# Performance work log

Measured on AMD Instinct MI355X. Metric: run time of the kernel, lower is better.

Reference implementation:

```python
import jax, jax.numpy as jnp
import numpy as np

B, S, D_MODEL, D_K, D_V = 8, 2048, 1024, 1024, 1024


def setup_inputs() -> dict:
    key = jax.random.key(0)
    ks = jax.random.split(key, 10)
    scale = 1.0 / np.sqrt(D_MODEL)
    return {
        "inputs_q": jax.random.normal(ks[0], (B, S, D_MODEL), dtype=jnp.float32),
        "inputs_k": jax.random.normal(ks[1], (B, S, D_MODEL), dtype=jnp.float32),
        "inputs_v": jax.random.normal(ks[2], (B, S, D_MODEL), dtype=jnp.float32),
        "mask": jax.random.randint(ks[3], (B, S), 0, 2, dtype=jnp.int32),
        "Wq": jax.random.normal(ks[4], (D_MODEL, D_K), dtype=jnp.float32) * scale,
        "bq": jnp.zeros((D_K,), dtype=jnp.float32),
        "Wk": jax.random.normal(ks[5], (D_MODEL, D_K), dtype=jnp.float32) * scale,
        "bk": jnp.zeros((D_K,), dtype=jnp.float32),
        "Wv": jax.random.normal(ks[6], (D_MODEL, D_V), dtype=jnp.float32) * scale,
        "bv": jnp.zeros((D_V,), dtype=jnp.float32),
    }


def reference(inputs_q, inputs_k, inputs_v, mask, Wq, bq, Wk, bk, Wv, bv):
    # Dense projections: [B,S,d_model] @ [d_model,d] + bias
    q = jnp.einsum("bsd,dk->bsk", inputs_q, Wq) + bq
    k = jnp.einsum("bsd,dk->bsk", inputs_k, Wk) + bk
    v = jnp.einsum("bsd,dv->bsv", inputs_v, Wv) + bv
    # scaled dot-product scores [B,S,S]
    scores = jnp.einsum("bqk,bsk->bqs", q, k) / jnp.sqrt(jnp.float32(D_K))
    # padding mask [B,S] -> matrix mask via min(row, col); 1 = valid
    m = mask.astype(jnp.float32)
    matrix_mask = jnp.minimum(m[:, :, None], m[:, None, :])  # [B,S,S]
    mask_float = 1.0 - matrix_mask  # 1 where masked
    scores = scores + mask_float * (-1e9)
    attention_weights = jax.nn.softmax(scores, axis=-1)
    out = jnp.einsum("bqs,bsv->bqv", attention_weights, v)  # [B,S,d_v]
    return out
```

## Files before the change

kernel.cpp:

```cpp
#include <hip/hip_runtime.h>
#include <stdint.h>


typedef unsigned short u16;
typedef __attribute__((ext_vector_type(8))) short short8;
typedef __attribute__((ext_vector_type(4))) float f32x4;

__device__ __forceinline__ u16 f2bf(float x) {
  unsigned u = __float_as_uint(x);
  return (u16)((u + 0x7FFFu + ((u >> 16) & 1u)) >> 16);
}
__device__ __forceinline__ float bf2f(u16 h) {
  return __uint_as_float(((unsigned)h) << 16);
}

__device__ __forceinline__ void stage16(const void* g, void* l) {
  const __attribute__((address_space(1))) uint32_t* gp =
      (const __attribute__((address_space(1))) uint32_t*)(uintptr_t)g;
  __attribute__((address_space(3))) uint32_t* lp =
      (__attribute__((address_space(3))) uint32_t*)(uintptr_t)l;
  __builtin_amdgcn_global_load_lds(gp, lp, 16, 0, 0);
}

__device__ __forceinline__ short8 ld8(const char* p, int off) {
  return *(const short8*)(p + off);
}

__global__ __launch_bounds__(256) void maskscan(const int* __restrict__ mask,
                                                int* __restrict__ idxA,
                                                int* __restrict__ nvA,
                                                int* __restrict__ nvp128A) {
  const int b = blockIdx.x;
  const int t = threadIdx.x, lane = t & 63, w = t >> 6;
  const int* m = mask + b * 2048;
  int v[8], loc = 0;
#pragma unroll
  for (int i = 0; i < 8; ++i) { v[i] = m[t * 8 + i]; loc += v[i]; }
  int sc = loc;
  for (int off = 1; off < 64; off <<= 1) {
    int n = __shfl_up(sc, off);
    if (lane >= off) sc += n;
  }
  __shared__ int wsum[4];
  if (lane == 63) wsum[w] = sc;
  __syncthreads();
  int woff = 0;
  for (int i = 0; i < w; ++i) woff += wsum[i];
  int pos = woff + sc - loc;
#pragma unroll
  for (int i = 0; i < 8; ++i)
    if (v[i]) idxA[b * 2048 + (pos++)] = t * 8 + i;
  if (t == 255) {
    const int nv = woff + sc;
    nvA[b] = nv;
    nvp128A[b] = (nv + 127) & ~127;
  }
}

__global__ __launch_bounds__(256) void compact3(const float* __restrict__ Xq,
                                                const float* __restrict__ Xk,
                                                const float* __restrict__ Xv,
                                                const int* __restrict__ idxA,
                                                const int* __restrict__ nvA,
                                                u16* __restrict__ Oq,
                                                u16* __restrict__ Ok,
                                                u16* __restrict__ Ov) {
  const int b = blockIdx.y, j = blockIdx.x, z = blockIdx.z;
  if (j >= nvA[b]) return;
  const float* X = (z == 0) ? Xq : (z == 1) ? Xk : Xv;
  u16* out = (z == 0) ? Oq : (z == 1) ? Ok : Ov;
  const int src = idxA[b * 2048 + j];
  const float4* s = (const float4*)(X + ((size_t)b * 2048 + src) * 1024);
  ushort4* d = (ushort4*)(out + ((size_t)b * 2048 + j) * 1024);
  const float4 f = s[threadIdx.x];
  ushort4 o;
  o.x = f2bf(f.x); o.y = f2bf(f.y); o.z = f2bf(f.z); o.w = f2bf(f.w);
  d[threadIdx.x] = o;
}

__global__ __launch_bounds__(256) void wtcol(const float* __restrict__ Wq,
                                             const float* __restrict__ Wk,
                                             const float* __restrict__ Wv,
                                             u16* __restrict__ WT,
                                             const float* __restrict__ Xv,
                                             float* __restrict__ partial) {
  const int bid = blockIdx.x;
  const int t = threadIdx.x;
  if (bid < 3072) {
    __shared__ float tile[32][33];
    const int z = bid >> 10;
    const int xy = bid & 1023;
    const int n0 = (xy & 31) * 32, d0 = (xy >> 5) * 32;
    const float* W = (z == 0) ? Wq : (z == 1) ? Wk : Wv;
    u16* out = WT + (size_t)z * 1024 * 1024;
    const int tx = t & 31, ty = t >> 5;
#pragma unroll
    for (int i = 0; i < 4; ++i)
      tile[ty + 8 * i][tx] = W[(size_t)(d0 + ty + 8 * i) * 1024 + n0 + tx];
    __syncthreads();
#pragma unroll
    for (int i = 0; i < 4; ++i)
      out[(size_t)(n0 + ty + 8 * i) * 1024 + d0 + tx] = f2bf(tile[tx][ty + 8 * i]);
  } else {
    const int r = bid - 3072;
    const int b = r & 7, dq = (r >> 3) & 3, sck = r >> 5;
    const int d = dq * 256 + t;
    const float* p = Xv + ((size_t)b * 2048 + sck * 256) * 1024 + d;
    float s0 = 0, s1 = 0, s2 = 0, s3 = 0;
    for (int rr = 0; rr < 256; rr += 4) {
      s0 += p[(size_t)(rr + 0) * 1024];
      s1 += p[(size_t)(rr + 1) * 1024];
      s2 += p[(size_t)(rr + 2) * 1024];
      s3 += p[(size_t)(rr + 3) * 1024];
    }
    partial[((size_t)b * 8 + sck) * 1024 + d] = (s0 + s1) + (s2 + s3);
  }
}

__global__ __launch_bounds__(256) void vpartk(const float* __restrict__ partial,
                                              const float* __restrict__ Wv,
                                              float* __restrict__ vpart) {
  const int b = blockIdx.x, cq = blockIdx.y, dk = blockIdx.z;
  const int t = threadIdx.x;
  __shared__ float mx[128];
  if (t < 128) {
    const int d = dk * 128 + t;
    float m = 0;
#pragma unroll
    for (int i = 0; i < 8; ++i) m += partial[((size_t)b * 8 + i) * 1024 + d];
    mx[t] = m * (1.0f / 2048.0f);
  }
  __syncthreads();
  const int c = cq * 256 + t;
  const float* wp = Wv + (size_t)(dk * 128) * 1024 + c;
  float acc = 0;
#pragma unroll 4
  for (int i = 0; i < 128; ++i) acc += mx[i] * wp[(size_t)i * 1024];
  vpart[((size_t)b * 8 + dk) * 1024 + c] = acc;
}

__global__ __launch_bounds__(256) void vmeanred(const float* __restrict__ vpart,
                                                const float* __restrict__ bv,
                                                float* __restrict__ vmean) {
  const int b = blockIdx.x;
  const int c = blockIdx.y * 256 + threadIdx.x;
  float acc = bv[c];
#pragma unroll
  for (int i = 0; i < 8; ++i) acc += vpart[((size_t)b * 8 + i) * 1024 + c];
  vmean[b * 1024 + c] = acc;
}

__global__ __launch_bounds__(256) void bcast(const int* __restrict__ mask,
                                             const float* __restrict__ vmean,
                                             float* __restrict__ out) {
  const int b = blockIdx.y, row = blockIdx.x;
  if (mask[b * 2048 + row] != 0) return;
  const float4 vv = ((const float4*)(vmean + b * 1024))[threadIdx.x];
  ((float4*)(out + ((size_t)b * 2048 + row) * 1024))[threadIdx.x] = vv;
}

#define BAR __builtin_amdgcn_s_barrier()
#define SB __builtin_amdgcn_sched_barrier(0)
#define LGK0 asm volatile("s_waitcnt lgkmcnt(0)" ::: "memory")
#define VM4 asm volatile("s_waitcnt vmcnt(4)" ::: "memory")
#define VM0 asm volatile("s_waitcnt vmcnt(0)" ::: "memory")

#define RDA4(P0, P1, MH)                                      \
  {                                                           \
    _Pragma("unroll") for (int mf_ = 0; mf_ < 4; ++mf_) {     \
      afr[0][mf_] = ld8(P0, (MH) * 8192 + mf_ * 2048);        \
      afr[1][mf_] = ld8(P1, (MH) * 8192 + mf_ * 2048);        \
    }                                                         \
  }

#define RDB2(DST, P0, P1, NH)                                 \
  {                                                           \
    DST[0][0] = ld8(P0, (NH) * 4096);                         \
    DST[0][1] = ld8(P0, (NH) * 4096 + 2048);                  \
    DST[1][0] = ld8(P1, (NH) * 4096);                         \
    DST[1][1] = ld8(P1, (NH) * 4096 + 2048);                  \
  }

#define MQ16(ACC, NH, BF)                                                \
  __builtin_amdgcn_s_setprio(1);                                         \
  {                                                                      \
    _Pragma("unroll") for (int ks_ = 0; ks_ < 2; ++ks_)                  \
        _Pragma("unroll") for (int mf_ = 0; mf_ < 4; ++mf_)              \
            _Pragma("unroll") for (int nf_ = 0; nf_ < 2; ++nf_)          \
                ACC[mf_][(NH) * 2 + nf_] =                               \
                    __builtin_amdgcn_mfma_f32_16x16x32_bf16(             \
                        afr[ks_][mf_], BF[ks_][nf_],                     \
                        ACC[mf_][(NH) * 2 + nf_], 0, 0, 0);              \
  }                                                                      \
  __builtin_amdgcn_s_setprio(0);

__global__ __launch_bounds__(512, 2) void gemm8p(
    const u16* __restrict__ A, const u16* __restrict__ B,
    void* __restrict__ C, void* __restrict__ C1, void* __restrict__ C2,
    const float* __restrict__ b0, const float* __restrict__ b1,
    const float* __restrict__ b2,
    const int* __restrict__ nvp128A,
    int K, int lda, int ldb, int ldc) {
  __shared__ __attribute__((aligned(16))) char smem[131072];
  const int tid = threadIdx.x;
  const int lane = tid & 63;
  const int w = tid >> 6;
  const int wr = w >> 2;
  const int wc = w & 3;

  const int bx = blockIdx.x;
  const int z = bx & 7;
  int r = bx >> 3;
  const int o = r >> 5; r &= 31;
  const int bm = r >> 2, bn = r & 3;

  const int nvp = nvp128A[z];
  if (bm * 256 >= nvp) return;

  const u16* Ap = A + (size_t)o * (8u * 2048u * 1024u) + (size_t)z * (2048u * 1024u);
  const u16* Bp = B + (size_t)o * (1024u * 1024u);
  const int half = K >> 7;

  const int srow = w * 8 + (lane >> 3);
  const int scol = ((lane & 7) ^ (lane >> 3)) << 3;
  const u16* Ab0 = Ap + (size_t)(bm * 256 + srow) * lda + scol;
  const u16* Ab1 = Ab0 + (size_t)64 * lda;
  const u16* Ab2 = Ab0 + (size_t)128 * lda;
  const u16* Ab3 = Ab0 + (size_t)192 * lda;
  const u16* Bb0 = Bp + (size_t)(bn * 256 + srow) * ldb + scol;
  const u16* Bb1 = Bb0 + (size_t)64 * ldb;
  const u16* Bb2 = Bb0 + (size_t)128 * ldb;
  const u16* Bb3 = Bb0 + (size_t)192 * ldb;
  char* ldsW = smem + w * 1024;

  const int fr = lane & 15;
  const int fq = lane >> 4;
  const int fx = (fr & 7) << 4;
  const char* pak0 = smem + wr * 16384 + fr * 128 + ((fq * 16) ^ fx);
  const char* pak1 = smem + wr * 16384 + fr * 128 + ((64 + fq * 16) ^ fx);
  const char* pak0b = pak0 + 65536;
  const char* pak1b = pak1 + 65536;
  const char* pbk0 = smem + 32768 + wc * 8192 + fr * 128 + ((fq * 16) ^ fx);
  const char* pbk1 = smem + 32768 + wc * 8192 + fr * 128 + ((64 + fq * 16) ^ fx);
  const char* pbk0b = pbk0 + 65536;
  const char* pbk1b = pbk1 + 65536;

  f32x4 acc0[4][4] = {};
  f32x4 acc1[4][4] = {};
  short8 afr[2][4], bf0[2][2], bf1[2][2];

  stage16(Bb0, ldsW + 32768); stage16(Bb1, ldsW + 40960);
  stage16(Bb2, ldsW + 49152); stage16(Bb3, ldsW + 57344);
  stage16(Ab0, ldsW + 0);     stage16(Ab1, ldsW + 8192);
  stage16(Ab2, ldsW + 16384); stage16(Ab3, ldsW + 24576);
  stage16(Bb0 + 64, ldsW + 98304);  stage16(Bb1 + 64, ldsW + 106496);
  stage16(Bb2 + 64, ldsW + 114688); stage16(Bb3 + 64, ldsW + 122880);
  VM4;
  BAR;

  int koff = 0;
  for (int i = 0; i < half - 1; ++i) {
    const int o1 = koff + 64, o2 = koff + 128, o3 = koff + 192;
    RDA4(pak0, pak1, 0); RDB2(bf0, pbk0, pbk1, 0);
    stage16(Ab0 + o1, ldsW + 65536); stage16(Ab1 + o1, ldsW + 73728);
    SB; BAR; LGK0; MQ16(acc0, 0, bf0); BAR;
    RDB2(bf1, pbk0, pbk1, 1);
    stage16(Ab2 + o1, ldsW + 81920); stage16(Ab3 + o1, ldsW + 90112);
    SB; BAR; LGK0; MQ16(acc0, 1, bf1); BAR;
    RDA4(pak0, pak1, 1);
    stage16(Bb0 + o2, ldsW + 32768); stage16(Bb1 + o2, ldsW + 40960);
    SB; BAR; LGK0; MQ16(acc1, 0, bf0); BAR;
    stage16(Bb2 + o2, ldsW + 49152); stage16(Bb3 + o2, ldsW + 57344);
    SB; BAR; MQ16(acc1, 1, bf1); VM4; BAR;
    RDA4(pak0b, pak1b, 0); RDB2(bf0, pbk0b, pbk1b, 0);
    stage16(Ab0 + o2, ldsW + 0); stage16(Ab1 + o2, ldsW + 8192);
    SB; BAR; LGK0; MQ16(acc0, 0, bf0); BAR;
    RDB2(bf1, pbk0b, pbk1b, 1);
    stage16(Ab2 + o2, ldsW + 16384); stage16(Ab3 + o2, ldsW + 24576);
    SB; BAR; LGK0; MQ16(acc0, 1, bf1); BAR;
    RDA4(pak0b, pak1b, 1);
    stage16(Bb0 + o3, ldsW + 98304); stage16(Bb1 + o3, ldsW + 106496);
    SB; BAR; LGK0; MQ16(acc1, 0, bf0); BAR;
    stage16(Bb2 + o3, ldsW + 114688); stage16(Bb3 + o3, ldsW + 122880);
    SB; BAR; MQ16(acc1, 1, bf1); VM4; BAR;
    koff += 128;
  }
  {
    const int o1 = koff + 64;
    RDA4(pak0, pak1, 0); RDB2(bf0, pbk0, pbk1, 0);
    stage16(Ab0 + o1, ldsW + 65536); stage16(Ab1 + o1, ldsW + 73728);
    SB; BAR; LGK0; MQ16(acc0, 0, bf0); BAR;
    RDB2(bf1, pbk0, pbk1, 1);
    stage16(Ab2 + o1, ldsW + 81920); stage16(Ab3 + o1, ldsW + 90112);
    SB; BAR; LGK0; MQ16(acc0, 1, bf1); BAR;
    RDA4(pak0, pak1, 1);
    SB; BAR; LGK0; MQ16(acc1, 0, bf0); BAR;
    SB; BAR; MQ16(acc1, 1, bf1); VM0; BAR;
    RDA4(pak0b, pak1b, 0); RDB2(bf0, pbk0b, pbk1b, 0);
    SB; BAR; LGK0; MQ16(acc0, 0, bf0); BAR;
    RDB2(bf1, pbk0b, pbk1b, 1);
    SB; BAR; LGK0; MQ16(acc0, 1, bf1); BAR;
    RDA4(pak0b, pak1b, 1);
    SB; BAR; LGK0; MQ16(acc1, 0, bf0); BAR;
    SB; BAR; MQ16(acc1, 1, bf1); BAR;
  }

  const int colb = bn * 256 + wc * 64 + fr;
#pragma unroll
  for (int mh = 0; mh < 2; ++mh) {
    f32x4(&ac)[4][4] = mh ? acc1 : acc0;
    const int rowl = bm * 256 + wr * 128 + mh * 64 + fq * 4;
    if (o < 2) {
      const float* bp = o ? b1 : b0;
      u16* Cb = (u16*)(o ? C1 : C) + (size_t)z * (2048u * 1024u);
#pragma unroll
      for (int mf = 0; mf < 4; ++mf)
#pragma unroll
        for (int n = 0; n < 4; ++n) {
          const int c = colb + n * 16;
          const float bv = bp[c];
#pragma unroll
          for (int j = 0; j < 4; ++j)
            Cb[(size_t)(rowl + mf * 16 + j) * ldc + c] = f2bf(ac[mf][n][j] + bv);
        }
    } else {
      u16* Cb = (u16*)C2;
#pragma unroll
      for (int mf = 0; mf < 4; ++mf) {
        const int s_ = rowl + mf * 16;
#pragma unroll
        for (int n = 0; n < 4; ++n) {
          const int c = colb + n * 16;
          const float bv = b2[c];
          ushort4 ov;
          ov.x = f2bf(ac[mf][n][0] + bv);
          ov.y = f2bf(ac[mf][n][1] + bv);
          ov.z = f2bf(ac[mf][n][2] + bv);
          ov.w = f2bf(ac[mf][n][3] + bv);
          *(ushort4*)&Cb[((size_t)z * 1024 + c) * 2048 + s_] = ov;
        }
      }
    }
  }
}

template <int MODE>
__global__ __launch_bounds__(256, 2) void gemm128(
    const u16* __restrict__ A, const u16* __restrict__ B, void* __restrict__ C,
    const int* __restrict__ nvp128A, const int* __restrict__ nvA,
    const int* __restrict__ idxA,
    int K, int lda, int ldb, int ldc,
    size_t Az, size_t Bz, size_t Cz) {
  __shared__ __attribute__((aligned(16))) u16 lsA[2 * 128 * 32];
  __shared__ __attribute__((aligned(16))) u16 lsB[2 * 128 * 32];
  const int tid = threadIdx.x;
  const int lane = tid & 63;
  const int w = tid >> 6;
  const int wr = w >> 1, wc = w & 1;

  const int bx = blockIdx.x;
  const int z = bx & 7;
  const int r = bx >> 3;
  int bm, bn;
  if constexpr (MODE == 2) { bm = r >> 4; bn = r & 15; }
  else                     { bm = r >> 3; bn = r & 7; }

  const int nvp = nvp128A[z];
  if (bm * 128 >= nvp) return;
  if constexpr (MODE == 2) { if (bn * 128 >= nvp) return; }
  const int Kz = (MODE == 3) ? nvp : K;

  const u16* Ap = A + (size_t)z * Az;
  const u16* Bp = B + (size_t)z * Bz;

  const int srow = lane >> 2;
  const int scol = (lane & 3) * 8;
  const u16* Ag0 = Ap + (size_t)(bm * 128 + w * 32 + srow) * lda + scol;
  const u16* Ag1 = Ag0 + (size_t)16 * lda;
  const u16* Bg0 = Bp + (size_t)(bn * 128 + w * 32 + srow) * ldb + scol;
  const u16* Bg1 = Bg0 + (size_t)16 * ldb;
  u16* lA0 = &lsA[(w * 32) * 32];
  u16* lA1 = &lsA[(w * 32 + 16) * 32];
  u16* lB0 = &lsB[(w * 32) * 32];
  u16* lB1 = &lsB[(w * 32 + 16) * 32];

  const int arow = wr * 64 + (lane & 15);
  const int brow = wc * 64 + (lane & 15);
  const int ko = (lane >> 4) * 8;

  f32x4 acc[4][4] = {};

  auto compute = [&](int cur) {
    const u16* sA = lsA + cur * 4096;
    const u16* sB = lsB + cur * 4096;
    short8 af[4], bfr[4];
#pragma unroll
    for (int m = 0; m < 4; ++m)
      af[m] = *(const short8*)&sA[(arow + m * 16) * 32 + ko];
#pragma unroll
    for (int n = 0; n < 4; ++n)
      bfr[n] = *(const short8*)&sB[(brow + n * 16) * 32 + ko];
#pragma unroll
    for (int m = 0; m < 4; ++m)
#pragma unroll
      for (int n = 0; n < 4; ++n)
        acc[m][n] =
            __builtin_amdgcn_mfma_f32_16x16x32_bf16(af[m], bfr[n], acc[m][n], 0, 0, 0);
  };

  stage16(Ag0, lA0);
  stage16(Ag1, lA1);
  stage16(Bg0, lB0);
  stage16(Bg1, lB1);
  __syncthreads();

  int cur = 0;
  int k0 = 0;
  for (; k0 + 32 < Kz; k0 += 32) {
    const int off = (cur ^ 1) * 4096;
    const int kn = k0 + 32;
    stage16(Ag0 + kn, lA0 + off);
    stage16(Ag1 + kn, lA1 + off);
    stage16(Bg0 + kn, lB0 + off);
    stage16(Bg1 + kn, lB1 + off);
    compute(cur);
    __syncthreads();
    cur ^= 1;
  }
  compute(cur);

  const int col0 = bn * 128 + wc * 64 + (lane & 15);
  const int row0 = bm * 128 + wr * 64 + ((lane >> 4) << 2);

  if constexpr (MODE == 2) {
    u16* Cb = (u16*)C + (size_t)z * Cz;
#pragma unroll
    for (int m = 0; m < 4; ++m)
#pragma unroll
      for (int n = 0; n < 4; ++n) {
        const int c = col0 + n * 16;
#pragma unroll
        for (int j = 0; j < 4; ++j)
          Cb[(size_t)(row0 + m * 16 + j) * ldc + c] =
              f2bf(acc[m][n][j] * 0.03125f);
      }
  } else {
    const int nv = nvA[z];
    const int* idxp = idxA + z * 2048;
    float* Ob = (float*)C;
#pragma unroll
    for (int m = 0; m < 4; ++m)
#pragma unroll
      for (int j = 0; j < 4; ++j) {
        const int rowc = row0 + m * 16 + j;
        if (rowc < nv) {
          const int gr = idxp[rowc];
          float* orow = Ob + ((size_t)z * 2048 + gr) * 1024;
#pragma unroll
          for (int n = 0; n < 4; ++n) orow[col0 + n * 16] = acc[m][n][j];
        }
      }
  }
}

__global__ __launch_bounds__(256) void softmaxc(u16* __restrict__ scores,
                                                const int* __restrict__ nvA,
                                                const int* __restrict__ nvp128A) {
  const int b = blockIdx.y, row = blockIdx.x;
  const int nv = nvA[b];
  if (row >= nv) return;
  const int nvp = nvp128A[b];
  const int t = threadIdx.x, lane = t & 63, w = t >> 6;
  u16* sc = scores + ((size_t)b * 2048 + row) * 2048;
  const int c0 = t * 8;
  float v[8];
  if (c0 < nvp) {
    const ushort4 h0 = *(const ushort4*)&sc[c0];
    const ushort4 h1 = *(const ushort4*)&sc[c0 + 4];
    v[0] = bf2f(h0.x); v[1] = bf2f(h0.y); v[2] = bf2f(h0.z); v[3] = bf2f(h0.w);
    v[4] = bf2f(h1.x); v[5] = bf2f(h1.y); v[6] = bf2f(h1.z); v[7] = bf2f(h1.w);
  } else {
#pragma unroll
    for (int i = 0; i < 8; ++i) v[i] = 0.f;
  }
  float lmax = -3.0e38f;
#pragma unroll
  for (int i = 0; i < 8; ++i)
    if (c0 + i < nv) lmax = fmaxf(lmax, v[i]);
#pragma unroll
  for (int off = 32; off >= 1; off >>= 1) lmax = fmaxf(lmax, __shfl_xor(lmax, off));
  __shared__ float red[8];
  if (lane == 0) red[w] = lmax;
  __syncthreads();
  const float bmax = fmaxf(fmaxf(red[0], red[1]), fmaxf(red[2], red[3]));
  float e[8];
  float lsum = 0.f;
#pragma unroll
  for (int i = 0; i < 8; ++i) {
    e[i] = (c0 + i < nv) ? __expf(v[i] - bmax) : 0.f;
    lsum += e[i];
  }
#pragma unroll
  for (int off = 32; off >= 1; off >>= 1) lsum += __shfl_xor(lsum, off);
  if (lane == 0) red[4 + w] = lsum;
  __syncthreads();
  const float inv = 1.0f / ((red[4] + red[5]) + (red[6] + red[7]));
  if (c0 < nvp) {
    ushort4 o0, o1;
    o0.x = f2bf(e[0] * inv); o0.y = f2bf(e[1] * inv);
    o0.z = f2bf(e[2] * inv); o0.w = f2bf(e[3] * inv);
    o1.x = f2bf(e[4] * inv); o1.y = f2bf(e[5] * inv);
    o1.z = f2bf(e[6] * inv); o1.w = f2bf(e[7] * inv);
    *(ushort4*)&sc[c0] = o0;
    *(ushort4*)&sc[c0 + 4] = o1;
  }
}

extern "C" void kernel_launch(void* const* d_in, const int* in_sizes, int n_in,
                              void* d_out, int out_size, void* d_ws, size_t ws_size,
                              hipStream_t stream) {
  const float* in_q = (const float*)d_in[0];
  const float* in_k = (const float*)d_in[1];
  const float* in_v = (const float*)d_in[2];
  const int* mask = (const int*)d_in[3];
  const float* Wq = (const float*)d_in[4];
  const float* bq = (const float*)d_in[5];
  const float* Wk = (const float*)d_in[6];
  const float* bk = (const float*)d_in[7];
  const float* Wv = (const float*)d_in[8];
  const float* bv = (const float*)d_in[9];

  char* ws = (char*)d_ws;
  const size_t SZ = (size_t)16384 * 1024 * 2;
  u16* qc = (u16*)(ws);
  u16* kc = (u16*)(ws + SZ);
  u16* vcT = (u16*)(ws + 2 * SZ);
  u16* Xc = (u16*)(ws + 3 * SZ);
  u16* Xqc = Xc;
  u16* Xkc = Xc + (size_t)8 * 2048 * 1024;
  u16* Xvc = Xkc + (size_t)8 * 2048 * 1024;
  u16* scores = (u16*)(ws + 3 * SZ);
  u16* WT = (u16*)(ws + 6 * SZ);
  char* misc = ws + 6 * SZ + 6 * 1024 * 1024;
  int* idxA = (int*)misc;
  int* nvA = idxA + 8 * 2048;
  int* nvp128A = nvA + 8;
  float* partial = (float*)(misc + 128 * 1024);
  float* vmean = (float*)(misc + 384 * 1024);
  float* vpart = (float*)(misc + 448 * 1024);

  maskscan<<<8, 256, 0, stream>>>(mask, idxA, nvA, nvp128A);

  compact3<<<dim3(2048, 8, 3), 256, 0, stream>>>(in_q, in_k, in_v, idxA, nvA,
                                                 Xqc, Xkc, Xvc);
  wtcol<<<3328, 256, 0, stream>>>(Wq, Wk, Wv, WT, in_v, partial);
  vpartk<<<dim3(8, 4, 8), 256, 0, stream>>>(partial, Wv, vpart);
  vmeanred<<<dim3(8, 4), 256, 0, stream>>>(vpart, bv, vmean);

  gemm8p<<<768, 512, 0, stream>>>(
      Xqc, WT, qc, kc, vcT, bq, bk, bv, nvp128A, 1024, 1024, 1024, 1024);

  gemm128<2><<<2048, 256, 0, stream>>>(
      qc, kc, scores, nvp128A, nvA, idxA, 1024, 1024, 1024, 2048,
      (size_t)2048 * 1024, (size_t)2048 * 1024, (size_t)2048 * 2048);

  softmaxc<<<dim3(2048, 8), 256, 0, stream>>>(scores, nvA, nvp128A);

  gemm128<3><<<1024, 256, 0, stream>>>(
      scores, vcT, d_out, nvp128A, nvA, idxA, 0, 2048, 2048, 1024,
      (size_t)2048 * 2048, (size_t)1024 * 2048, 0);

  bcast<<<dim3(2048, 8), 256, 0, stream>>>(mask, vmean, (float*)d_out);
}
```

Baseline: 252.3 us.

## Fold small side kernels into neighboring launches to cut launch count

Result: faster. 230.6 us (-8.6%).

```diff
diff --git a/kernel.cpp b/kernel.cpp
--- a/kernel.cpp
+++ b/kernel.cpp
@@ -26,70 +26,49 @@
   return *(const short8*)(p + off);
 }
 
-__global__ __launch_bounds__(256) void maskscan(const int* __restrict__ mask,
-                                                int* __restrict__ idxA,
-                                                int* __restrict__ nvA,
-                                                int* __restrict__ nvp128A) {
-  const int b = blockIdx.x;
-  const int t = threadIdx.x, lane = t & 63, w = t >> 6;
-  const int* m = mask + b * 2048;
-  int v[8], loc = 0;
-#pragma unroll
-  for (int i = 0; i < 8; ++i) { v[i] = m[t * 8 + i]; loc += v[i]; }
-  int sc = loc;
-  for (int off = 1; off < 64; off <<= 1) {
-    int n = __shfl_up(sc, off);
-    if (lane >= off) sc += n;
-  }
+__global__ __launch_bounds__(256) void scanwt(const int* __restrict__ mask,
+                                              int* __restrict__ idxA,
+                                              int* __restrict__ nvA,
+                                              int* __restrict__ nvp128A,
+                                              const float* __restrict__ Wq,
+                                              const float* __restrict__ Wk,
+                                              const float* __restrict__ Wv,
+                                              u16* __restrict__ WT,
+                                              const float* __restrict__ Xv,
+                                              float* __restrict__ partial) {
   __shared__ int wsum[4];
-  if (lane == 63) wsum[w] = sc;
-  __syncthreads();
-  int woff = 0;
-  for (int i = 0; i < w; ++i) woff += wsum[i];
-  int pos = woff + sc - loc;
-#pragma unroll
-  for (int i = 0; i < 8; ++i)
-    if (v[i]) idxA[b * 2048 + (pos++)] = t * 8 + i;
-  if (t == 255) {
-    const int nv = woff + sc;
-    nvA[b] = nv;
-    nvp128A[b] = (nv + 127) & ~127;
-  }
-}
-
-__global__ __launch_bounds__(256) void compact3(const float* __restrict__ Xq,
-                                                const float* __restrict__ Xk,
-                                                const float* __restrict__ Xv,
-                                                const int* __restrict__ idxA,
-                                                const int* __restrict__ nvA,
-                                                u16* __restrict__ Oq,
-                                                u16* __restrict__ Ok,
-                                                u16* __restrict__ Ov) {
-  const int b = blockIdx.y, j = blockIdx.x, z = blockIdx.z;
-  if (j >= nvA[b]) return;
-  const float* X = (z == 0) ? Xq : (z == 1) ? Xk : Xv;
-  u16* out = (z == 0) ? Oq : (z == 1) ? Ok : Ov;
-  const int src = idxA[b * 2048 + j];
-  const float4* s = (const float4*)(X + ((size_t)b * 2048 + src) * 1024);
-  ushort4* d = (ushort4*)(out + ((size_t)b * 2048 + j) * 1024);
-  const float4 f = s[threadIdx.x];
-  ushort4 o;
-  o.x = f2bf(f.x); o.y = f2bf(f.y); o.z = f2bf(f.z); o.w = f2bf(f.w);
-  d[threadIdx.x] = o;
-}
-
-__global__ __launch_bounds__(256) void wtcol(const float* __restrict__ Wq,
-                                             const float* __restrict__ Wk,
-                                             const float* __restrict__ Wv,
-                                             u16* __restrict__ WT,
-                                             const float* __restrict__ Xv,
-                                             float* __restrict__ partial) {
+  __shared__ float tile[32][33];
   const int bid = blockIdx.x;
   const int t = threadIdx.x;
-  if (bid < 3072) {
-    __shared__ float tile[32][33];
-    const int z = bid >> 10;
-    const int xy = bid & 1023;
+  if (bid < 8) {
+    const int b = bid;
+    const int lane = t & 63, w = t >> 6;
+    const int* m = mask + b * 2048;
+    int v[8], loc = 0;
+#pragma unroll
+    for (int i = 0; i < 8; ++i) { v[i] = m[t * 8 + i]; loc += v[i]; }
+    int sc = loc;
+    for (int off = 1; off < 64; off <<= 1) {
+      int n = __shfl_up(sc, off);
+      if (lane >= off) sc += n;
+    }
+    if (lane == 63) wsum[w] = sc;
+    __syncthreads();
+    int woff = 0;
+    for (int i = 0; i < w; ++i) woff += wsum[i];
+    int pos = woff + sc - loc;
+#pragma unroll
+    for (int i = 0; i < 8; ++i)
+      if (v[i]) idxA[b * 2048 + (pos++)] = t * 8 + i;
+    if (t == 255) {
+      const int nv = woff + sc;
+      nvA[b] = nv;
+      nvp128A[b] = (nv + 127) & ~127;
+    }
+  } else if (bid < 3080) {
+    const int q = bid - 8;
+    const int z = q >> 10;
+    const int xy = q & 1023;
     const int n0 = (xy & 31) * 32, d0 = (xy >> 5) * 32;
     const float* W = (z == 0) ? Wq : (z == 1) ? Wk : Wv;
     u16* out = WT + (size_t)z * 1024 * 1024;
@@ -102,7 +81,7 @@
     for (int i = 0; i < 4; ++i)
       out[(size_t)(n0 + ty + 8 * i) * 1024 + d0 + tx] = f2bf(tile[tx][ty + 8 * i]);
   } else {
-    const int r = bid - 3072;
+    const int r = bid - 3080;
     const int b = r & 7, dq = (r >> 3) & 3, sck = r >> 5;
     const int d = dq * 256 + t;
     const float* p = Xv + ((size_t)b * 2048 + sck * 256) * 1024 + d;
@@ -117,46 +96,30 @@
   }
 }
 
-__global__ __launch_bounds__(256) void vpartk(const float* __restrict__ partial,
-                                              const float* __restrict__ Wv,
-                                              float* __restrict__ vpart) {
-  const int b = blockIdx.x, cq = blockIdx.y, dk = blockIdx.z;
-  const int t = threadIdx.x;
-  __shared__ float mx[128];
-  if (t < 128) {
-    const int d = dk * 128 + t;
-    float m = 0;
-#pragma unroll
-    for (int i = 0; i < 8; ++i) m += partial[((size_t)b * 8 + i) * 1024 + d];
-    mx[t] = m * (1.0f / 2048.0f);
-  }
-  __syncthreads();
-  const int c = cq * 256 + t;
-  const float* wp = Wv + (size_t)(dk * 128) * 1024 + c;
-  float acc = 0;
-#pragma unroll 4
-  for (int i = 0; i < 128; ++i) acc += mx[i] * wp[(size_t)i * 1024];
-  vpart[((size_t)b * 8 + dk) * 1024 + c] = acc;
-}
-
-__global__ __launch_bounds__(256) void vmeanred(const float* __restrict__ vpart,
-                                                const float* __restrict__ bv,
-                                                float* __restrict__ vmean) {
-  const int b = blockIdx.x;
-  const int c = blockIdx.y * 256 + threadIdx.x;
-  float acc = bv[c];
-#pragma unroll
-  for (int i = 0; i < 8; ++i) acc += vpart[((size_t)b * 8 + i) * 1024 + c];
-  vmean[b * 1024 + c] = acc;
-}
-
-__global__ __launch_bounds__(256) void bcast(const int* __restrict__ mask,
-                                             const float* __restrict__ vmean,
-                                             float* __restrict__ out) {
-  const int b = blockIdx.y, row = blockIdx.x;
-  if (mask[b * 2048 + row] != 0) return;
-  const float4 vv = ((const float4*)(vmean + b * 1024))[threadIdx.x];
-  ((float4*)(out + ((size_t)b * 2048 + row) * 1024))[threadIdx.x] = vv;
+__global__ __launch_bounds__(256) void compact3(const float* __restrict__ Xq,
+                                                const float* __restrict__ Xk,
+                                                const float* __restrict__ Xv,
+                                                const int* __restrict__ idxA,
+                                                const int* __restrict__ nvA,
+                                                u16* __restrict__ Oq,
+                                                u16* __restrict__ Ok,
+                                                u16* __restrict__ Ov) {
+  const int b = blockIdx.y, z = blockIdx.z;
+  const int w = threadIdx.x >> 6, lane = threadIdx.x & 63;
+  const int j = blockIdx.x * 4 + w;
+  if (j >= nvA[b]) return;
+  const float* X = (z == 0) ? Xq : (z == 1) ? Xk : Xv;
+  u16* out = (z == 0) ? Oq : (z == 1) ? Ok : Ov;
+  const int src = idxA[b * 2048 + j];
+  const float4* s = (const float4*)(X + ((size_t)b * 2048 + src) * 1024);
+  ushort4* d = (ushort4*)(out + ((size_t)b * 2048 + j) * 1024);
+#pragma unroll
+  for (int p = 0; p < 4; ++p) {
+    const float4 f = s[lane + p * 64];
+    ushort4 o;
+    o.x = f2bf(f.x); o.y = f2bf(f.y); o.z = f2bf(f.z); o.w = f2bf(f.w);
+    d[lane + p * 64] = o;
+  }
 }
 
 #define BAR __builtin_amdgcn_s_barrier()
@@ -200,8 +163,33 @@
     const float* __restrict__ b0, const float* __restrict__ b1,
     const float* __restrict__ b2,
     const int* __restrict__ nvp128A,
+    const float* __restrict__ partial, const float* __restrict__ WvF,
+    float* __restrict__ vpart,
     int K, int lda, int ldb, int ldc) {
   __shared__ __attribute__((aligned(16))) char smem[131072];
+
+  if (blockIdx.x >= 768) {
+    float* mx = (float*)smem;
+    const int r2 = blockIdx.x - 768;
+    const int b = r2 & 7, cq = (r2 >> 3) & 1, dk = r2 >> 4;
+    const int t = threadIdx.x;
+    if (t < 128) {
+      const int d = dk * 128 + t;
+      float m = 0;
+#pragma unroll
+      for (int i = 0; i < 8; ++i) m += partial[((size_t)b * 8 + i) * 1024 + d];
+      mx[t] = m * (1.0f / 2048.0f);
+    }
+    __syncthreads();
+    const int c = cq * 512 + t;
+    const float* wp = WvF + (size_t)(dk * 128) * 1024 + c;
+    float acc = 0;
+#pragma unroll 4
+    for (int i = 0; i < 128; ++i) acc += mx[i] * wp[(size_t)i * 1024];
+    vpart[((size_t)b * 8 + dk) * 1024 + c] = acc;
+    return;
+  }
+
   const int tid = threadIdx.x;
   const int lane = tid & 63;
   const int w = tid >> 6;
@@ -349,10 +337,26 @@
     const u16* __restrict__ A, const u16* __restrict__ B, void* __restrict__ C,
     const int* __restrict__ nvp128A, const int* __restrict__ nvA,
     const int* __restrict__ idxA,
+    const float* __restrict__ p0, const float* __restrict__ p1,
+    float* __restrict__ p2,
     int K, int lda, int ldb, int ldc,
     size_t Az, size_t Bz, size_t Cz) {
   __shared__ __attribute__((aligned(16))) u16 lsA[2 * 128 * 32];
   __shared__ __attribute__((aligned(16))) u16 lsB[2 * 128 * 32];
+
+  if constexpr (MODE == 2) {
+    if (blockIdx.x >= 2048) {
+      const int r2 = blockIdx.x - 2048;
+      const int b = r2 & 7, cq = r2 >> 3;
+      const int c = cq * 256 + threadIdx.x;
+      float acc = p1[c];
+#pragma unroll
+      for (int i = 0; i < 8; ++i) acc += p0[((size_t)b * 8 + i) * 1024 + c];
+      p2[b * 1024 + c] = acc;
+      return;
+    }
+  }
+
   const int tid = threadIdx.x;
   const int lane = tid & 63;
   const int w = tid >> 6;
@@ -463,10 +467,19 @@
   }
 }
 
-__global__ __launch_bounds__(256) void softmaxc(u16* __restrict__ scores,
-                                                const int* __restrict__ nvA,
-                                                const int* __restrict__ nvp128A) {
+__global__ __launch_bounds__(256) void softbc(u16* __restrict__ scores,
+                                              const int* __restrict__ nvA,
+                                              const int* __restrict__ nvp128A,
+                                              const int* __restrict__ mask,
+                                              const float* __restrict__ vmean,
+                                              float* __restrict__ out) {
   const int b = blockIdx.y, row = blockIdx.x;
+  if (blockIdx.z == 1) {
+    if (mask[b * 2048 + row] != 0) return;
+    const float4 vv = ((const float4*)(vmean + b * 1024))[threadIdx.x];
+    ((float4*)(out + ((size_t)b * 2048 + row) * 1024))[threadIdx.x] = vv;
+    return;
+  }
   const int nv = nvA[b];
   if (row >= nv) return;
   const int nvp = nvp128A[b];
@@ -549,26 +562,26 @@
   float* vmean = (float*)(misc + 384 * 1024);
   float* vpart = (float*)(misc + 448 * 1024);
 
-  maskscan<<<8, 256, 0, stream>>>(mask, idxA, nvA, nvp128A);
-
-  compact3<<<dim3(2048, 8, 3), 256, 0, stream>>>(in_q, in_k, in_v, idxA, nvA,
-                                                 Xqc, Xkc, Xvc);
-  wtcol<<<3328, 256, 0, stream>>>(Wq, Wk, Wv, WT, in_v, partial);
-  vpartk<<<dim3(8, 4, 8), 256, 0, stream>>>(partial, Wv, vpart);
-  vmeanred<<<dim3(8, 4), 256, 0, stream>>>(vpart, bv, vmean);
-
-  gemm8p<<<768, 512, 0, stream>>>(
-      Xqc, WT, qc, kc, vcT, bq, bk, bv, nvp128A, 1024, 1024, 1024, 1024);
-
-  gemm128<2><<<2048, 256, 0, stream>>>(
-      qc, kc, scores, nvp128A, nvA, idxA, 1024, 1024, 1024, 2048,
+  scanwt<<<3336, 256, 0, stream>>>(mask, idxA, nvA, nvp128A, Wq, Wk, Wv, WT,
+                                   in_v, partial);
+
+  compact3<<<dim3(512, 8, 3), 256, 0, stream>>>(in_q, in_k, in_v, idxA, nvA,
+                                                Xqc, Xkc, Xvc);
+
+  gemm8p<<<896, 512, 0, stream>>>(
+      Xqc, WT, qc, kc, vcT, bq, bk, bv, nvp128A, partial, Wv, vpart,
+      1024, 1024, 1024, 1024);
+
+  gemm128<2><<<2080, 256, 0, stream>>>(
+      qc, kc, scores, nvp128A, nvA, idxA, vpart, bv, vmean,
+      1024, 1024, 1024, 2048,
       (size_t)2048 * 1024, (size_t)2048 * 1024, (size_t)2048 * 2048);
 
-  softmaxc<<<dim3(2048, 8), 256, 0, stream>>>(scores, nvA, nvp128A);
+  softbc<<<dim3(2048, 8, 2), 256, 0, stream>>>(scores, nvA, nvp128A, mask,
+                                               vmean, (float*)d_out);
 
   gemm128<3><<<1024, 256, 0, stream>>>(
-      scores, vcT, d_out, nvp128A, nvA, idxA, 0, 2048, 2048, 1024,
+      scores, vcT, d_out, nvp128A, nvA, idxA, nullptr, nullptr, nullptr,
+      0, 2048, 2048, 1024,
       (size_t)2048 * 2048, (size_t)1024 * 2048, 0);
-
-  bcast<<<dim3(2048, 8), 256, 0, stream>>>(mask, vmean, (float*)d_out);
-}
+}
```
